# Optimization experiments

Hardware: AMD Instinct MI355X
Metric: run time of the kernel (lower is better)

Reference implementation:

```python
import jax, jax.numpy as jnp
import numpy as np

HID = [512, 256, 128, 32]
VOCAB = 41
LATENT = 512
SOS = 1


def setup_inputs() -> dict:
    key = jax.random.key(0)
    ks = jax.random.split(key, 16)
    B, S = 1024, 350
    inp = {
        'latent': jax.random.normal(ks[0], (B, LATENT), dtype=jnp.float32),
        'target_tokens': jax.random.randint(ks[1], (B, S), 0, VOCAB),
    }
    def lin(k, out_d, in_d):
        s = 1.0 / np.sqrt(in_d)
        return jax.random.uniform(k, (out_d, in_d), jnp.float32, -s, s)
    # token_embedding: Linear(vocab -> 512)
    inp['W_emb'] = lin(ks[2], HID[0], VOCAB)
    inp['b_emb'] = jnp.zeros((HID[0],), jnp.float32)
    # init_state: Linear(latent -> 256+128+32)
    inp['W_init'] = lin(ks[3], sum(HID[1:]), LATENT)
    inp['b_init'] = jnp.zeros((sum(HID[1:]),), jnp.float32)
    # 3 GRUCells: (in, hid) = (512,256), (256,128), (128,32)
    for i in range(3):
        in_d, h_d = HID[i], HID[i + 1]
        inp[f'Wih{i}'] = lin(ks[4 + 4 * i], 3 * h_d, in_d)
        inp[f'Whh{i}'] = lin(ks[5 + 4 * i], 3 * h_d, h_d)
        inp[f'bih{i}'] = jnp.zeros((3 * h_d,), jnp.float32)
        inp[f'bhh{i}'] = jnp.zeros((3 * h_d,), jnp.float32)
    # projection: Linear(32 -> vocab)
    inp['W_proj'] = lin(ks[15], VOCAB, HID[-1])
    inp['b_proj'] = jnp.zeros((VOCAB,), jnp.float32)
    return inp


def _gru_cell(x, h, Wih, Whh, bih, bhh):
    # PyTorch GRUCell math
    gi = x @ Wih.T + bih
    gh = h @ Whh.T + bhh
    ir, iz, inn = jnp.split(gi, 3, axis=-1)
    hr, hz, hn = jnp.split(gh, 3, axis=-1)
    r = jax.nn.sigmoid(ir + hr)
    z = jax.nn.sigmoid(iz + hz)
    n = jnp.tanh(inn + r * hn)
    return (1.0 - z) * n + z * h


def _forward(latent, target_tokens, W_emb, b_emb, W_init, b_init,
             Wih0, Whh0, bih0, bhh0, Wih1, Whh1, bih1, bhh1,
             Wih2, Whh2, bih2, bhh2, W_proj, b_proj):
    B, S = target_tokens.shape
    combined = latent @ W_init.T + b_init                 # [B, 416]
    h0 = combined[:, :HID[1]]
    h1 = combined[:, HID[1]:HID[1] + HID[2]]
    h2 = combined[:, HID[1] + HID[2]:]
    # token_embedding(one_hot(tok)) == W_emb[:, tok].T + b_emb -> precompute table
    emb_table = W_emb.T + b_emb                           # [vocab, 512]
    # teacher forcing: input at t=0 is SOS, at t>0 is target_tokens[:, t]
    toks = jnp.concatenate(
        [jnp.full((1, B), SOS, target_tokens.dtype), target_tokens.T[1:]], axis=0)  # [S, B]

    def step(carry, tok_t):
        h0, h1, h2 = carry
        x = emb_table[tok_t]                              # [B, 512]
        h0 = _gru_cell(x, h0, Wih0, Whh0, bih0, bhh0)
        h1 = _gru_cell(h0, h1, Wih1, Whh1, bih1, bhh1)
        h2 = _gru_cell(h1, h2, Wih2, Whh2, bih2, bhh2)
        logits = h2 @ W_proj.T + b_proj                   # [B, vocab]
        return (h0, h1, h2), logits

    _, logits_seq = jax.lax.scan(step, (h0, h1, h2), toks)  # [S, B, vocab]
    outputs = jnp.transpose(logits_seq, (1, 0, 2))          # [B, S, vocab]
    predicted = jnp.argmax(outputs, axis=-1).astype(jnp.float32)
    return outputs, predicted


def reference(latent, target_tokens, W_emb, b_emb, W_init, b_init,
              Wih0, Whh0, bih0, bhh0, Wih1, Whh1, bih1, bhh1,
              Wih2, Whh2, bih2, bhh2, W_proj, b_proj):
    return _forward(latent, target_tokens, W_emb, b_emb, W_init, b_init,
                    Wih0, Whh0, bih0, bhh0, Wih1, Whh1, bih1, bhh1,
                    Wih2, Whh2, bih2, bhh2, W_proj, b_proj)
```

## Files before the change

kernel.cpp:

```cpp
#include <hip/hip_runtime.h>
#include <hip/hip_bf16.h>

#define BATCH 1024
#define SEQ   350
#define LAT   512
#define VOC   41
#define H0D   512
#define H1D   256
#define H2D   128
#define H3D   32
#define G1    768
#define G2    384
#define G3    96
#define SOS   1

#define O_HH0   0
#define O_IH1   196608
#define O_HH1   294912
#define O_IH2   344064
#define O_HH2   356352
#define O_PROJ  359424
#define O_TAB   360736
#define WS_FLOATS 392224

#define RT 4
#define NT 512

__global__ void setup_kernel(const float* __restrict__ Whh0, const float* __restrict__ Wih1,
                             const float* __restrict__ Whh1, const float* __restrict__ Wih2,
                             const float* __restrict__ Whh2, const float* __restrict__ Wproj,
                             const float* __restrict__ Wemb, const float* __restrict__ bemb,
                             const float* __restrict__ Wih0, const float* __restrict__ bih0,
                             float* __restrict__ ws) {
  int idx = blockIdx.x * blockDim.x + threadIdx.x;
  if (idx < 196608) { int o = idx % G1, k = idx / G1; ws[O_HH0 + k*G1 + o] = Whh0[o*H1D + k]; return; }
  idx -= 196608;
  if (idx < 98304)  { int o = idx % G2, k = idx / G2; ws[O_IH1 + k*G2 + o] = Wih1[o*H1D + k]; return; }
  idx -= 98304;
  if (idx < 49152)  { int o = idx % G2, k = idx / G2; ws[O_HH1 + k*G2 + o] = Whh1[o*H2D + k]; return; }
  idx -= 49152;
  if (idx < 12288)  { int o = idx % G3, k = idx / G3; ws[O_IH2 + k*G3 + o] = Wih2[o*H2D + k]; return; }
  idx -= 12288;
  if (idx < 3072)   { int o = idx % G3, k = idx / G3; ws[O_HH2 + k*G3 + o] = Whh2[o*H3D + k]; return; }
  idx -= 3072;
  if (idx < 1312)   { int o = idx % VOC, k = idx / VOC; ws[O_PROJ + k*VOC + o] = Wproj[o*H3D + k]; return; }
  idx -= 1312;
  if (idx < 31488) {
    int o = idx % G1, v = idx / G1;
    double acc = (double)bih0[o];
    const float* wrow = Wih0 + (size_t)o * H0D;
    for (int k = 0; k < H0D; ++k)
      acc += ((double)Wemb[k*VOC + v] + (double)bemb[k]) * (double)wrow[k];
    ws[O_TAB + v*G1 + o] = (float)acc;
  }
}

__device__ __forceinline__ float sigf(float x) { return 1.0f / (1.0f + expf(-x)); }

__global__ __launch_bounds__(NT, 2) void gru_persist(
    const float* __restrict__ latent, const int* __restrict__ tgt,
    const float* __restrict__ Winit, const float* __restrict__ binit,
    const float* __restrict__ bhh0,
    const float* __restrict__ bih1, const float* __restrict__ bhh1,
    const float* __restrict__ bih2, const float* __restrict__ bhh2,
    const float* __restrict__ bproj,
    const float* __restrict__ ws, float* __restrict__ out)
{
  const int tid = threadIdx.x;
  const int r0 = blockIdx.x * RT;

  const float* wt_hh0 = ws + O_HH0;
  const float* wt_ih1 = ws + O_IH1;
  const float* wt_hh1 = ws + O_HH1;
  const float* wt_ih2 = ws + O_IH2;
  const float* wt_hh2 = ws + O_HH2;
  const float* wt_proj = ws + O_PROJ;
  const float* tab = ws + O_TAB;

  float* __restrict__ out_logits = out;
  float* __restrict__ out_pred = out + (size_t)BATCH * SEQ * VOC;

  __shared__ __align__(16) float h0s[RT][H1D];
  __shared__ __align__(16) float h1s[RT][H2D];
  __shared__ __align__(16) float h2s[RT][H3D];
  __shared__ float scA[2][RT][3][H1D];
  __shared__ float scBi[2][RT][3][H2D];
  __shared__ float scBh[2][RT][3][H2D];
  __shared__ float scC[10][3][RT][H3D];
  __shared__ float projS[H3D * VOC];
  __shared__ int   toksAll[RT][SEQ];

  const int j  = tid & 255;
  const int kh = tid >> 8;
  const int jb = tid & 127;
  const int g  = tid >> 7;
  const int jc = tid & 31;
  const int sc = tid >> 5;
  const int wv = tid >> 6;
  const int lane = tid & 63;

  const float bA_r = bhh0[j], bA_z = bhh0[256 + j], bA_n = bhh0[512 + j];
  const float bB_ir = bih1[jb], bB_iz = bih1[128 + jb], bB_in = bih1[256 + jb];
  const float bB_hr = bhh1[jb], bB_hz = bhh1[128 + jb], bB_hn = bhh1[256 + jb];
  const int jj2 = lane & 31;
  const float bC_ir = bih2[jj2], bC_iz = bih2[32 + jj2], bC_in = bih2[64 + jj2];
  const float bC_hr = bhh2[jj2], bC_hz = bhh2[32 + jj2], bC_hn = bhh2[64 + jj2];
  const int cpr = (lane < VOC) ? lane : 0;
  const float bP = bproj[cpr];

  for (int i = tid; i < RT * SEQ; i += NT) {
    int r = i / SEQ, tt = i - r * SEQ;
    toksAll[r][tt] = (tt == 0) ? SOS : tgt[(size_t)(r0 + r) * SEQ + tt];
  }
  for (int i = tid; i < H3D * VOC; i += NT) projS[i] = wt_proj[i];

  for (int idx = tid; idx < RT * 416; idx += NT) {
    int r = idx / 416, jj = idx - r * 416;
    const float* lrow = latent + (size_t)(r0 + r) * LAT;
    const float* wrow = Winit + (size_t)jj * LAT;
    double acc = (double)binit[jj];
    for (int k = 0; k < LAT; ++k) acc += (double)lrow[k] * (double)wrow[k];
    float a = (float)acc;
    if (jj < H1D) h0s[r][jj] = a;
    else if (jj < H1D + H2D) h1s[r][jj - H1D] = a;
    else h2s[r][jj - H1D - H2D] = a;
  }
  __syncthreads();

  for (int t = 0; t < SEQ; ++t) {
    {
      const int er0 = 2 * kh, er1 = er0 + 1;
      const float* trow0 = tab + (size_t)toksAll[er0][t] * G1;
      const float* trow1 = tab + (size_t)toksAll[er1][t] * G1;
      const float tv0x = trow0[j], tv0y = trow0[256 + j], tv0z = trow0[512 + j];
      const float tv1x = trow1[j], tv1y = trow1[256 + j], tv1z = trow1[512 + j];

      float aR[RT], aZ[RT], aN[RT];
      #pragma unroll
      for (int r = 0; r < RT; ++r) { aR[r] = 0.0f; aZ[r] = 0.0f; aN[r] = 0.0f; }
      const float* __restrict__ wbase = wt_hh0 + j;
      const int k0 = kh * 128;
      for (int kb = k0; kb < k0 + 128; kb += 4) {
        float4 hv[RT];
        #pragma unroll
        for (int r = 0; r < RT; ++r) hv[r] = *(const float4*)&h0s[r][kb];
        #pragma unroll
        for (int u = 0; u < 4; ++u) {
          const float* wp = wbase + (size_t)(kb + u) * G1;
          const float wr = wp[0], wz = wp[256], wn = wp[512];
          #pragma unroll
          for (int r = 0; r < RT; ++r) {
            const float hval = ((const float*)&hv[r])[u];
            aR[r] = fmaf(hval, wr, aR[r]);
            aZ[r] = fmaf(hval, wz, aZ[r]);
            aN[r] = fmaf(hval, wn, aN[r]);
          }
        }
      }
      #pragma unroll
      for (int r = 0; r < RT; ++r) {
        scA[kh][r][0][j] = aR[r];
        scA[kh][r][1][j] = aZ[r];
        scA[kh][r][2][j] = aN[r];
      }
      __syncthreads();
      {
        const int oth = 1 - kh;
        #pragma unroll
        for (int e = 0; e < 2; ++e) {
          const int r = er0 + e;
          const float tx = e ? tv1x : tv0x;
          const float ty = e ? tv1y : tv0y;
          const float tz = e ? tv1z : tv0z;
          const float gR  = tx + aR[r] + scA[oth][r][0][j] + bA_r;
          const float gZ  = ty + aZ[r] + scA[oth][r][1][j] + bA_z;
          const float ghN =      aN[r] + scA[oth][r][2][j] + bA_n;
          const float rg = sigf(gR);
          const float zg = sigf(gZ);
          const float ng = tanhf(fmaf(rg, ghN, tz));
          h0s[r][j] = (1.0f - zg) * ng + zg * h0s[r][j];
        }
      }
    }
    __syncthreads();

    {
      float bR[RT], bZ[RT], bN[RT];
      #pragma unroll
      for (int r = 0; r < RT; ++r) { bR[r] = 0.0f; bZ[r] = 0.0f; bN[r] = 0.0f; }
      if (g < 2) {
        const float* __restrict__ wbase = wt_ih1 + jb;
        const int k0 = g * 128;
        for (int kb = k0; kb < k0 + 128; kb += 4) {
          float4 hv[RT];
          #pragma unroll
          for (int r = 0; r < RT; ++r) hv[r] = *(const float4*)&h0s[r][kb];
          #pragma unroll
          for (int u = 0; u < 4; ++u) {
            const float* wp = wbase + (size_t)(kb + u) * G2;
            const float wr = wp[0], wz = wp[128], wn = wp[256];
            #pragma unroll
            for (int r = 0; r < RT; ++r) {
              const float hval = ((const float*)&hv[r])[u];
              bR[r] = fmaf(hval, wr, bR[r]);
              bZ[r] = fmaf(hval, wz, bZ[r]);
              bN[r] = fmaf(hval, wn, bN[r]);
            }
          }
        }
        #pragma unroll
        for (int r = 0; r < RT; ++r) {
          scBi[g][r][0][jb] = bR[r];
          scBi[g][r][1][jb] = bZ[r];
          scBi[g][r][2][jb] = bN[r];
        }
      } else {
        const float* __restrict__ wbase = wt_hh1 + jb;
        const int k0 = (g - 2) * 64;
        for (int kb = k0; kb < k0 + 64; kb += 4) {
          float4 hv[RT];
          #pragma unroll
          for (int r = 0; r < RT; ++r) hv[r] = *(const float4*)&h1s[r][kb];
          #pragma unroll
          for (int u = 0; u < 4; ++u) {
            const float* wp = wbase + (size_t)(kb + u) * G2;
            const float wr = wp[0], wz = wp[128], wn = wp[256];
            #pragma unroll
            for (int r = 0; r < RT; ++r) {
              const float hval = ((const float*)&hv[r])[u];
              bR[r] = fmaf(hval, wr, bR[r]);
              bZ[r] = fmaf(hval, wz, bZ[r]);
              bN[r] = fmaf(hval, wn, bN[r]);
            }
          }
        }
        #pragma unroll
        for (int r = 0; r < RT; ++r) {
          scBh[g - 2][r][0][jb] = bR[r];
          scBh[g - 2][r][1][jb] = bZ[r];
          scBh[g - 2][r][2][jb] = bN[r];
        }
      }
      __syncthreads();
      if (g >= 2) {
        const int rb = (g - 2) * 2;
        const int oh = 3 - g;
        #pragma unroll
        for (int e = 0; e < 2; ++e) {
          const int r = rb + e;
          const float giR = scBi[0][r][0][jb] + scBi[1][r][0][jb] + bB_ir;
          const float giZ = scBi[0][r][1][jb] + scBi[1][r][1][jb] + bB_iz;
          const float giN = scBi[0][r][2][jb] + scBi[1][r][2][jb] + bB_in;
          const float ghR = bR[r] + scBh[oh][r][0][jb] + bB_hr;
          const float ghZ = bZ[r] + scBh[oh][r][1][jb] + bB_hz;
          const float ghN = bN[r] + scBh[oh][r][2][jb] + bB_hn;
          const float rg = sigf(giR + ghR);
          const float zg = sigf(giZ + ghZ);
          const float ng = tanhf(fmaf(rg, ghN, giN));
          h1s[r][jb] = (1.0f - zg) * ng + zg * h1s[r][jb];
        }
      }
    }
    __syncthreads();

    {
      float cR[RT], cZ[RT], cN[RT];
      #pragma unroll
      for (int r = 0; r < RT; ++r) { cR[r] = 0.0f; cZ[r] = 0.0f; cN[r] = 0.0f; }
      if (sc < 8) {
        for (int kk = 0; kk < 16; ++kk) {
          int k = sc * 16 + kk;
          const float* wp = wt_ih2 + (size_t)k * G3;
          const float wr = wp[jc], wz = wp[32 + jc], wn = wp[64 + jc];
          #pragma unroll
          for (int r = 0; r < RT; ++r) {
            const float hval = h1s[r][k];
            cR[r] = fmaf(hval, wr, cR[r]);
            cZ[r] = fmaf(hval, wz, cZ[r]);
            cN[r] = fmaf(hval, wn, cN[r]);
          }
        }
      } else if (sc < 10) {
        for (int kk = 0; kk < 16; ++kk) {
          int k = (sc - 8) * 16 + kk;
          const float* wp = wt_hh2 + (size_t)k * G3;
          const float wr = wp[jc], wz = wp[32 + jc], wn = wp[64 + jc];
          #pragma unroll
          for (int r = 0; r < RT; ++r) {
            const float hval = h2s[r][k];
            cR[r] = fmaf(hval, wr, cR[r]);
            cZ[r] = fmaf(hval, wz, cZ[r]);
            cN[r] = fmaf(hval, wn, cN[r]);
          }
        }
      }
      if (sc < 10) {
        #pragma unroll
        for (int r = 0; r < RT; ++r) {
          scC[sc][0][r][jc] = cR[r];
          scC[sc][1][r][jc] = cZ[r];
          scC[sc][2][r][jc] = cN[r];
        }
      }
    }
    __syncthreads();

    if (wv < 4) {
      const int r = wv;
      float h2f = 0.0f;
      if (lane < 32) {
        const int jj = lane;
        float giR = bC_ir, giZ = bC_iz, giN = bC_in;
        #pragma unroll
        for (int s = 0; s < 8; ++s) {
          giR += scC[s][0][r][jj];
          giZ += scC[s][1][r][jj];
          giN += scC[s][2][r][jj];
        }
        const float ghR = scC[8][0][r][jj] + scC[9][0][r][jj] + bC_hr;
        const float ghZ = scC[8][1][r][jj] + scC[9][1][r][jj] + bC_hz;
        const float ghN = scC[8][2][r][jj] + scC[9][2][r][jj] + bC_hn;
        const float rg = sigf(giR + ghR);
        const float zg = sigf(giZ + ghZ);
        const float ng = tanhf(fmaf(rg, ghN, giN));
        h2f = (1.0f - zg) * ng + zg * h2s[r][jj];
        h2s[r][jj] = h2f;
      }
      float acc = bP;
      #pragma unroll
      for (int k = 0; k < H3D; ++k) {
        const float hk = __shfl(h2f, k);
        acc = fmaf(hk, projS[k * VOC + cpr], acc);
      }
      if (lane < VOC)
        out_logits[((size_t)(r0 + r) * SEQ + t) * VOC + lane] = acc;
      float val = (lane < VOC) ? acc : -3.402823466e38f;
      int idx = lane;
      #pragma unroll
      for (int off = 32; off > 0; off >>= 1) {
        const float ov = __shfl_xor(val, off);
        const int   oi = __shfl_xor(idx, off);
        if (ov > val || (ov == val && oi < idx)) { val = ov; idx = oi; }
      }
      if (lane == 0)
        out_pred[(size_t)(r0 + r) * SEQ + t] = (float)idx;
    }
  }
}

extern "C" void kernel_launch(void* const* d_in, const int* in_sizes, int n_in,
                              void* d_out, int out_size, void* d_ws, size_t ws_size,
                              hipStream_t stream) {
  const float* latent  = (const float*)d_in[0];
  const int*   tgt     = (const int*)d_in[1];
  const float* Wemb    = (const float*)d_in[2];
  const float* bemb    = (const float*)d_in[3];
  const float* Winit   = (const float*)d_in[4];
  const float* binit   = (const float*)d_in[5];
  const float* Wih0    = (const float*)d_in[6];
  const float* Whh0    = (const float*)d_in[7];
  const float* bih0    = (const float*)d_in[8];
  const float* bhh0    = (const float*)d_in[9];
  const float* Wih1    = (const float*)d_in[10];
  const float* Whh1    = (const float*)d_in[11];
  const float* bih1    = (const float*)d_in[12];
  const float* bhh1    = (const float*)d_in[13];
  const float* Wih2    = (const float*)d_in[14];
  const float* Whh2    = (const float*)d_in[15];
  const float* bih2    = (const float*)d_in[16];
  const float* bhh2    = (const float*)d_in[17];
  const float* Wproj   = (const float*)d_in[18];
  const float* bproj   = (const float*)d_in[19];

  float* ws = (float*)d_ws;
  float* out = (float*)d_out;

  int setup_threads = WS_FLOATS;
  int setup_blocks = (setup_threads + 255) / 256;
  setup_kernel<<<setup_blocks, 256, 0, stream>>>(Whh0, Wih1, Whh1, Wih2, Whh2, Wproj,
                                                Wemb, bemb, Wih0, bih0, ws);

  gru_persist<<<BATCH / RT, NT, 0, stream>>>(latent, tgt, Winit, binit,
                                             bhh0, bih1, bhh1, bih2, bhh2, bproj,
                                             ws, out);
}
```

Before: 6.786 ms.

## Split layer-0 K reduction within wavefront and double-buffer h0 to drop a barrier

Layer 0's two K-halves now sit in the two 32-lane halves of the same wavefront instead of in separate thread halves. The partial sums are combined with __shfl_xor, which removes the scA shared-memory scratch and one __syncthreads per timestep. h0 is double-buffered, so the epilogue can write the new state without racing with reads of the old state. Each thread now covers a different j/k mapping, which may change global weight-load coalescing, since each half-wave now reads only 32 contiguous columns.

```diff
diff --git a/kernel.cpp b/kernel.cpp
--- a/kernel.cpp
+++ b/kernel.cpp
@@ -68,6 +68,8 @@
 {
   const int tid = threadIdx.x;
   const int r0 = blockIdx.x * RT;
+  const int lane = tid & 63;
+  const int wv = tid >> 6;
 
   const float* wt_hh0 = ws + O_HH0;
   const float* wt_ih1 = ws + O_IH1;
@@ -80,26 +82,25 @@
   float* __restrict__ out_logits = out;
   float* __restrict__ out_pred = out + (size_t)BATCH * SEQ * VOC;
 
-  __shared__ __align__(16) float h0s[RT][H1D];
+  __shared__ __align__(16) float h0s[2][RT][H1D];
   __shared__ __align__(16) float h1s[RT][H2D];
   __shared__ __align__(16) float h2s[RT][H3D];
-  __shared__ float scA[2][RT][3][H1D];
   __shared__ float scBi[2][RT][3][H2D];
   __shared__ float scBh[2][RT][3][H2D];
   __shared__ float scC[10][3][RT][H3D];
   __shared__ float projS[H3D * VOC];
   __shared__ int   toksAll[RT][SEQ];
 
-  const int j  = tid & 255;
-  const int kh = tid >> 8;
+  const int jA  = (wv << 5) + (lane & 31);
+  const int kh  = lane >> 5;
+  const int kA0 = kh << 7;
+  const int rbA = kh << 1;
   const int jb = tid & 127;
   const int g  = tid >> 7;
   const int jc = tid & 31;
   const int sc = tid >> 5;
-  const int wv = tid >> 6;
-  const int lane = tid & 63;
-
-  const float bA_r = bhh0[j], bA_z = bhh0[256 + j], bA_n = bhh0[512 + j];
+
+  const float bA_r = bhh0[jA], bA_z = bhh0[256 + jA], bA_n = bhh0[512 + jA];
   const float bB_ir = bih1[jb], bB_iz = bih1[128 + jb], bB_in = bih1[256 + jb];
   const float bB_hr = bhh1[jb], bB_hz = bhh1[128 + jb], bB_hn = bhh1[256 + jb];
   const int jj2 = lane & 31;
@@ -121,29 +122,29 @@
     double acc = (double)binit[jj];
     for (int k = 0; k < LAT; ++k) acc += (double)lrow[k] * (double)wrow[k];
     float a = (float)acc;
-    if (jj < H1D) h0s[r][jj] = a;
+    if (jj < H1D) h0s[0][r][jj] = a;
     else if (jj < H1D + H2D) h1s[r][jj - H1D] = a;
     else h2s[r][jj - H1D - H2D] = a;
   }
   __syncthreads();
 
+  int cur0 = 0;
+
   for (int t = 0; t < SEQ; ++t) {
     {
-      const int er0 = 2 * kh, er1 = er0 + 1;
-      const float* trow0 = tab + (size_t)toksAll[er0][t] * G1;
-      const float* trow1 = tab + (size_t)toksAll[er1][t] * G1;
-      const float tv0x = trow0[j], tv0y = trow0[256 + j], tv0z = trow0[512 + j];
-      const float tv1x = trow1[j], tv1y = trow1[256 + j], tv1z = trow1[512 + j];
+      const float* trow0 = tab + (size_t)toksAll[rbA][t] * G1;
+      const float* trow1 = tab + (size_t)toksAll[rbA + 1][t] * G1;
+      const float t0x = trow0[jA], t0y = trow0[256 + jA], t0z = trow0[512 + jA];
+      const float t1x = trow1[jA], t1y = trow1[256 + jA], t1z = trow1[512 + jA];
 
       float aR[RT], aZ[RT], aN[RT];
       #pragma unroll
       for (int r = 0; r < RT; ++r) { aR[r] = 0.0f; aZ[r] = 0.0f; aN[r] = 0.0f; }
-      const float* __restrict__ wbase = wt_hh0 + j;
-      const int k0 = kh * 128;
-      for (int kb = k0; kb < k0 + 128; kb += 4) {
+      const float* __restrict__ wbase = wt_hh0 + jA;
+      for (int kb = kA0; kb < kA0 + 128; kb += 4) {
         float4 hv[RT];
         #pragma unroll
-        for (int r = 0; r < RT; ++r) hv[r] = *(const float4*)&h0s[r][kb];
+        for (int r = 0; r < RT; ++r) hv[r] = *(const float4*)&h0s[cur0][r][kb];
         #pragma unroll
         for (int u = 0; u < 4; ++u) {
           const float* wp = wbase + (size_t)(kb + u) * G1;
@@ -157,30 +158,31 @@
           }
         }
       }
+      float oR[RT], oZ[RT], oN[RT];
       #pragma unroll
       for (int r = 0; r < RT; ++r) {
-        scA[kh][r][0][j] = aR[r];
-        scA[kh][r][1][j] = aZ[r];
-        scA[kh][r][2][j] = aN[r];
-      }
-      __syncthreads();
-      {
-        const int oth = 1 - kh;
-        #pragma unroll
-        for (int e = 0; e < 2; ++e) {
-          const int r = er0 + e;
-          const float tx = e ? tv1x : tv0x;
-          const float ty = e ? tv1y : tv0y;
-          const float tz = e ? tv1z : tv0z;
-          const float gR  = tx + aR[r] + scA[oth][r][0][j] + bA_r;
-          const float gZ  = ty + aZ[r] + scA[oth][r][1][j] + bA_z;
-          const float ghN =      aN[r] + scA[oth][r][2][j] + bA_n;
-          const float rg = sigf(gR);
-          const float zg = sigf(gZ);
-          const float ng = tanhf(fmaf(rg, ghN, tz));
-          h0s[r][j] = (1.0f - zg) * ng + zg * h0s[r][j];
-        }
-      }
+        oR[r] = __shfl_xor(aR[r], 32);
+        oZ[r] = __shfl_xor(aZ[r], 32);
+        oN[r] = __shfl_xor(aN[r], 32);
+      }
+#define EPIA(r, tx, ty, tz)                                                \
+      {                                                                    \
+        const float gR  = tx + aR[r] + oR[r] + bA_r;                       \
+        const float gZ  = ty + aZ[r] + oZ[r] + bA_z;                       \
+        const float ghN =      aN[r] + oN[r] + bA_n;                       \
+        const float rg = sigf(gR);                                         \
+        const float zg = sigf(gZ);                                         \
+        const float ng = tanhf(fmaf(rg, ghN, tz));                         \
+        h0s[cur0 ^ 1][r][jA] = (1.0f - zg) * ng + zg * h0s[cur0][r][jA];   \
+      }
+      if (lane < 32) {
+        EPIA(0, t0x, t0y, t0z)
+        EPIA(1, t1x, t1y, t1z)
+      } else {
+        EPIA(2, t0x, t0y, t0z)
+        EPIA(3, t1x, t1y, t1z)
+      }
+#undef EPIA
     }
     __syncthreads();
 
@@ -194,7 +196,7 @@
         for (int kb = k0; kb < k0 + 128; kb += 4) {
           float4 hv[RT];
           #pragma unroll
-          for (int r = 0; r < RT; ++r) hv[r] = *(const float4*)&h0s[r][kb];
+          for (int r = 0; r < RT; ++r) hv[r] = *(const float4*)&h0s[cur0 ^ 1][r][kb];
           #pragma unroll
           for (int u = 0; u < 4; ++u) {
             const float* wp = wbase + (size_t)(kb + u) * G2;
@@ -345,6 +347,7 @@
       if (lane == 0)
         out_pred[(size_t)(r0 + r) * SEQ + t] = (float)idx;
     }
+    cur0 ^= 1;
   }
 }
 
```

Result: no change. 6.778 ms (-0.1%).
